# Kernel tuning notes

Measured on AMD Instinct MI355X. Metric: run time of the kernel, lower is better.

Reference implementation:

```python
import jax, jax.numpy as jnp
import numpy as np

B, C, D, O = 4, 4096, 1024, 1024
PROJ = 256
RANKS = [1, 2, 4, 8]
E = len(RANKS)
CLAMP_MAX = float(np.log(1.0 / 0.01))  # log(100)


def setup_inputs() -> dict:
    key = jax.random.key(0)
    ks = jax.random.split(key, 16)
    inp = {
        "x": jax.random.normal(ks[0], (B, C, D), dtype=jnp.float32),
        "W": jax.random.normal(ks[1], (O, D), dtype=jnp.float32) / np.sqrt(D),
        "Wp": jax.random.normal(ks[2], (PROJ, D), dtype=jnp.float32) / np.sqrt(D),
        "bp": jnp.zeros((PROJ,), dtype=jnp.float32),
        "sim": jax.random.normal(ks[3], (PROJ, E), dtype=jnp.float32) * 0.01,
        "temp": jnp.full((1,), np.log(1.0 / 0.5), dtype=jnp.float32),
    }
    for i, r in enumerate(RANKS):
        inp[f"Wd{i}"] = jax.random.normal(ks[4 + 2 * i], (r, D), dtype=jnp.float32) / r
        inp[f"Wu{i}"] = jax.random.normal(ks[5 + 2 * i], (O, r), dtype=jnp.float32) * 0.01
    return inp


def _l2norm(v, axis):
    return v / jnp.maximum(jnp.linalg.norm(v, axis=axis, keepdims=True), 1e-12)


def reference(x, W, Wp, bp, sim, temp, Wd0, Wu0, Wd1, Wu1, Wd2, Wu2, Wd3, Wu3):
    # base linear (bias=False)
    base = jnp.einsum("bcd,od->bco", x, W)

    # cosine top-k gate on flattened tokens
    xf = x.reshape(-1, x.shape[-1])                         # [N, D]
    proj = _l2norm(xf @ Wp.T + bp, axis=1)                  # [N, PROJ]
    simn = _l2norm(sim, axis=0)                             # [PROJ, E]
    scale = jnp.exp(jnp.minimum(temp, CLAMP_MAX))
    logits = (proj @ simn) * scale                          # [N, E]

    # eval mode: no noise. softmax then top-1 mask * prob
    lw = jax.nn.softmax(logits, axis=1)
    top1 = jnp.argmax(lw, axis=1)                           # [N]
    ret = jnp.where(jnp.arange(E)[None, :] == top1[:, None], lw, 0.0)
    ret = ret.reshape(x.shape[0], x.shape[1], E)            # [B, C, E]

    # dense per-expert LoRA (ranks differ, so small fixed loop)
    downs = (Wd0, Wd1, Wd2, Wd3)
    ups = (Wu0, Wu1, Wu2, Wu3)
    l = jnp.stack(
        [jnp.einsum("bcr,or->bco", jnp.einsum("bcd,rd->bcr", x, d), u)
         for d, u in zip(downs, ups)],
        axis=2,
    )                                                       # [B, C, E, O]
    res = jnp.sum(ret[..., None] * l, axis=2)               # [B, C, O]
    return base + res
```

## Files before the change

kernel.cpp:

```cpp
#include <hip/hip_runtime.h>

#define TOK 16384
#define DD 1024
#define OO 1024
#define KE 1088
#define NT 17
#define NB1 288
#define CLAMPV 4.605170185988091f

typedef __attribute__((ext_vector_type(8))) short short8;
typedef __attribute__((ext_vector_type(4))) float f32x4;

__device__ __forceinline__ unsigned short f2bf(float f) {
  unsigned int u = __float_as_uint(f);
  return (unsigned short)((u + 0x7FFFu + ((u >> 16) & 1u)) >> 16);
}

__device__ __forceinline__ void gload16(const unsigned short* g, unsigned short* l) {
  __builtin_amdgcn_global_load_lds(
      (const __attribute__((address_space(1))) void*)g,
      (__attribute__((address_space(3))) void*)l, 16, 0, 0);
}

__device__ __forceinline__ float down_val(int j, int d,
    const float* __restrict__ Wd0, const float* __restrict__ Wd1,
    const float* __restrict__ Wd2, const float* __restrict__ Wd3) {
  if (j == 0) return Wd0[d];
  if (j < 3) return Wd1[(j - 1) * DD + d];
  if (j < 7) return Wd2[(j - 3) * DD + d];
  if (j < 15) return Wd3[(j - 7) * DD + d];
  return 0.f;
}

__global__ __launch_bounds__(256) void prep3(
    const float* __restrict__ W, const float* __restrict__ Wp,
    const float* __restrict__ sim, const float* __restrict__ bp,
    const float* __restrict__ Wd0, const float* __restrict__ Wd1,
    const float* __restrict__ Wd2, const float* __restrict__ Wd3,
    const float* __restrict__ Wu0, const float* __restrict__ Wu1,
    const float* __restrict__ Wu2, const float* __restrict__ Wu3,
    unsigned short* __restrict__ Bx, unsigned short* __restrict__ B1,
    unsigned short* __restrict__ Ax, float* __restrict__ v4,
    float* __restrict__ c4) {
  __shared__ float simn_l[256][4];
  __shared__ float part[4][4];
  const int tid = threadIdx.x;
  if (blockIdx.x < 4) {
    float4 sv = *(const float4*)&sim[tid * 4];
    float v[4] = {sv.x * sv.x, sv.y * sv.y, sv.z * sv.z, sv.w * sv.w};
#pragma unroll
    for (int off = 1; off < 64; off <<= 1) {
#pragma unroll
      for (int e = 0; e < 4; ++e) v[e] += __shfl_xor(v[e], off, 64);
    }
    int wv = tid >> 6, ln = tid & 63;
    if (ln == 0) { part[wv][0] = v[0]; part[wv][1] = v[1]; part[wv][2] = v[2]; part[wv][3] = v[3]; }
    __syncthreads();
    float n0 = fmaxf(sqrtf(part[0][0] + part[1][0] + part[2][0] + part[3][0]), 1e-12f);
    float n1 = fmaxf(sqrtf(part[0][1] + part[1][1] + part[2][1] + part[3][1]), 1e-12f);
    float n2 = fmaxf(sqrtf(part[0][2] + part[1][2] + part[2][2] + part[3][2]), 1e-12f);
    float n3 = fmaxf(sqrtf(part[0][3] + part[1][3] + part[2][3] + part[3][3]), 1e-12f);
    simn_l[tid][0] = sv.x / n0; simn_l[tid][1] = sv.y / n1;
    simn_l[tid][2] = sv.z / n2; simn_l[tid][3] = sv.w / n3;
    __syncthreads();
    int d = blockIdx.x * 256 + tid;
    float a0 = 0.f, a1 = 0.f, a2 = 0.f, a3 = 0.f;
    for (int j = 0; j < 256; ++j) {
      float w = Wp[j * DD + d];
      a0 = __builtin_fmaf(w, simn_l[j][0], a0);
      a1 = __builtin_fmaf(w, simn_l[j][1], a1);
      a2 = __builtin_fmaf(w, simn_l[j][2], a2);
      a3 = __builtin_fmaf(w, simn_l[j][3], a3);
    }
    v4[d] = a0; v4[1024 + d] = a1; v4[2048 + d] = a2; v4[3072 + d] = a3;
    if (blockIdx.x == 0) {
      float bpv = bp[tid];
      float pc[4] = {simn_l[tid][0] * bpv, simn_l[tid][1] * bpv,
                     simn_l[tid][2] * bpv, simn_l[tid][3] * bpv};
#pragma unroll
      for (int off = 1; off < 64; off <<= 1) {
#pragma unroll
        for (int e = 0; e < 4; ++e) pc[e] += __shfl_xor(pc[e], off, 64);
      }
      __syncthreads();
      if (ln == 0) { part[wv][0] = pc[0]; part[wv][1] = pc[1]; part[wv][2] = pc[2]; part[wv][3] = pc[3]; }
      __syncthreads();
      if (tid == 0) {
#pragma unroll
        for (int e = 0; e < 4; ++e)
          c4[e] = part[0][e] + part[1][e] + part[2][e] + part[3][e];
      }
    }
  }
  const int nB1 = NB1 * DD;
  const int nWb = OO * KE;
  const int nXpad = TOK * 48;
  const int total = nB1 + nWb + nXpad;
  for (int i = blockIdx.x * 256 + tid; i < total; i += gridDim.x * 256) {
    if (i < nB1) {
      int r = i >> 10, c = i & 1023;
      float v = 0.f;
      if (r < 256) v = Wp[r * DD + c];
      else if (r < 271) v = down_val(r - 256, c, Wd0, Wd1, Wd2, Wd3);
      B1[i] = f2bf(v);
    } else if (i < nB1 + nWb) {
      int j = i - nB1;
      int o = j / KE, c = j - o * KE;
      float v = 0.f;
      if (c < 1024) v = W[o * DD + c];
      else if (c == 1024) v = Wu0[o];
      else if (c < 1027) v = Wu1[o * 2 + (c - 1025)];
      else if (c < 1031) v = Wu2[o * 4 + (c - 1027)];
      else if (c < 1039) v = Wu3[o * 8 + (c - 1031)];
      Bx[j] = f2bf(v);
    } else {
      int j = i - nB1 - nWb;
      int row = j / 48, c = j - row * 48;
      Ax[row * KE + 1040 + c] = 0;
    }
  }
}

__global__ __launch_bounds__(512, 1) void gemm2f(
    const float* __restrict__ x, const float* __restrict__ v4,
    unsigned short* __restrict__ Ax, const unsigned short* __restrict__ B1,
    const float* __restrict__ c4, const float* __restrict__ bp,
    const float* __restrict__ temp) {
  __shared__ __align__(16) unsigned short as1[2][64 * 32];
  __shared__ __align__(16) unsigned short bs1[2][NB1 * 32];
  __shared__ float ssq_s[2][64];
  __shared__ float xdown_s[64][16];
  __shared__ __align__(16) float dots_s[64][4];
  const int tid = threadIdx.x;
  const int lane = tid & 63, wv = tid >> 6;
  const int wm = wv >> 1, wn = wv & 1;
  const int r0 = blockIdx.x * 64;
  const int ro = lane & 15, ko = (lane >> 4) * 8;
  const int srow = lane >> 2, scol = (lane & 3) * 8;
  const int xr = tid >> 3;
  const int xc = (tid & 7) * 4;
  const float* xgp = &x[(r0 + xr) * DD + xc];
  unsigned short* axp = &Ax[(r0 + xr) * KE + xc];
  f32x4 acc[9] = {};
  float dotp[4] = {};
  float4 xv, va, vb, vc, vd;
  float4 xn, na, nb, nc, nd;

#define STB1(KT, BUF)                                                         \
  for (int c = wv; c < 18; c += 8)                                            \
    gload16(&B1[(c * 16 + srow) * DD + (KT) * 32 + scol], &bs1[BUF][c * 512]);

#define LOADX(KT, X, VA, VB, VC, VD) do {                                     \
    X  = *(const float4*)(xgp + (KT) * 32);                                   \
    VA = *(const float4*)&v4[(KT) * 32 + xc];                                 \
    VB = *(const float4*)&v4[1024 + (KT) * 32 + xc];                          \
    VC = *(const float4*)&v4[2048 + (KT) * 32 + xc];                          \
    VD = *(const float4*)&v4[3072 + (KT) * 32 + xc];                          \
  } while (0)

#define PROC(KT, BUF) do {                                                    \
    dotp[0] = __builtin_fmaf(xv.x, va.x, __builtin_fmaf(xv.y, va.y,           \
              __builtin_fmaf(xv.z, va.z, __builtin_fmaf(xv.w, va.w, dotp[0])))); \
    dotp[1] = __builtin_fmaf(xv.x, vb.x, __builtin_fmaf(xv.y, vb.y,           \
              __builtin_fmaf(xv.z, vb.z, __builtin_fmaf(xv.w, vb.w, dotp[1])))); \
    dotp[2] = __builtin_fmaf(xv.x, vc.x, __builtin_fmaf(xv.y, vc.y,           \
              __builtin_fmaf(xv.z, vc.z, __builtin_fmaf(xv.w, vc.w, dotp[2])))); \
    dotp[3] = __builtin_fmaf(xv.x, vd.x, __builtin_fmaf(xv.y, vd.y,           \
              __builtin_fmaf(xv.z, vd.z, __builtin_fmaf(xv.w, vd.w, dotp[3])))); \
    union { unsigned short s[4]; uint2 q; } pk;                               \
    pk.s[0] = f2bf(xv.x); pk.s[1] = f2bf(xv.y);                               \
    pk.s[2] = f2bf(xv.z); pk.s[3] = f2bf(xv.w);                               \
    *reinterpret_cast<uint2*>(axp + (KT) * 32) = pk.q;                        \
    *reinterpret_cast<uint2*>(&as1[BUF][xr * 32 + xc]) = pk.q;                \
  } while (0)

#define MM(BUF) do {                                                          \
    const unsigned short* ap = &as1[BUF][0];                                  \
    const unsigned short* bpp = &bs1[BUF][0];                                 \
    short8 af = *reinterpret_cast<const short8*>(ap + (wm * 16 + ro) * 32 + ko); \
    _Pragma("unroll")                                                         \
    for (int n = 0; n < 9; ++n) {                                             \
      short8 bf = *reinterpret_cast<const short8*>(                           \
          bpp + (wn * 144 + n * 16 + ro) * 32 + ko);                          \
      acc[n] = __builtin_amdgcn_mfma_f32_16x16x32_bf16(af, bf, acc[n], 0, 0, 0); \
    }                                                                         \
  } while (0)

  LOADX(0, xv, va, vb, vc, vd);
  STB1(0, 0)
  __builtin_amdgcn_sched_barrier(0);
  PROC(0, 0);
  LOADX(1, xn, na, nb, nc, nd);
  asm volatile("s_waitcnt vmcnt(6) lgkmcnt(0)" ::: "memory");
  __builtin_amdgcn_s_barrier();
  xv = xn; va = na; vb = nb; vc = nc; vd = nd;

  for (int u = 0; u < 32; ++u) {
    const int cb = u & 1;
    if (u < 31) {
      STB1(u + 1, cb ^ 1)
      __builtin_amdgcn_sched_barrier(0);
      PROC(u + 1, cb ^ 1);
      if (u < 30) LOADX(u + 2, xn, na, nb, nc, nd);
    }
    MM(cb);
    if (u < 31) {
      if (u < 30) {
        asm volatile("s_waitcnt vmcnt(6) lgkmcnt(0)" ::: "memory");
      } else {
        asm volatile("s_waitcnt vmcnt(1) lgkmcnt(0)" ::: "memory");
      }
      __builtin_amdgcn_s_barrier();
      xv = xn; va = na; vb = nb; vc = nc; vd = nd;
    }
  }

#pragma unroll
  for (int off = 1; off < 8; off <<= 1) {
#pragma unroll
    for (int e = 0; e < 4; ++e) dotp[e] += __shfl_xor(dotp[e], off, 64);
  }
  if ((lane & 7) == 0) {
    dots_s[xr][0] = dotp[0]; dots_s[xr][1] = dotp[1];
    dots_s[xr][2] = dotp[2]; dots_s[xr][3] = dotp[3];
  }

  float ssqp[4] = {};
#pragma unroll
  for (int n = 0; n < 9; ++n) {
    int col = wn * 144 + n * 16 + ro;
    if (col < 256) {
      float b = bp[col];
#pragma unroll
      for (int r = 0; r < 4; ++r) {
        float a = acc[n][r] + b;
        ssqp[r] = __builtin_fmaf(a, a, ssqp[r]);
      }
    }
  }
#pragma unroll
  for (int off = 1; off < 16; off <<= 1) {
#pragma unroll
    for (int r = 0; r < 4; ++r) ssqp[r] += __shfl_xor(ssqp[r], off, 64);
  }
  if (ro == 0) {
#pragma unroll
    for (int r = 0; r < 4; ++r)
      ssq_s[wn][wm * 16 + (lane >> 4) * 4 + r] = ssqp[r];
  }
  if (wn == 1 && ro < 15) {
#pragma unroll
    for (int r = 0; r < 4; ++r)
      xdown_s[wm * 16 + (lane >> 4) * 4 + r][ro] = acc[7][r];
  }
  __syncthreads();

  if (tid < 64) {
    const int row = tid, t = r0 + row;
    float ssqT = ssq_s[0][row] + ssq_s[1][row];
    float4 cc = *reinterpret_cast<const float4*>(c4);
    float scale = expf(fminf(temp[0], CLAMPV));
    float inv = scale / fmaxf(sqrtf(ssqT), 1e-12f);
    float l[4];
    l[0] = (dots_s[row][0] + cc.x) * inv; l[1] = (dots_s[row][1] + cc.y) * inv;
    l[2] = (dots_s[row][2] + cc.z) * inv; l[3] = (dots_s[row][3] + cc.w) * inv;
    int be = 0; float m = l[0];
    if (l[1] > m) { m = l[1]; be = 1; }
    if (l[2] > m) { m = l[2]; be = 2; }
    if (l[3] > m) { m = l[3]; be = 3; }
    float den = expf(l[0] - m) + expf(l[1] - m) + expf(l[2] - m) + expf(l[3] - m);
    float g = 1.0f / den;
    int off = (1 << be) - 1;
    int rr = 1 << be;
    union { unsigned short s[16]; uint4 v[2]; } o;
#pragma unroll
    for (int j = 0; j < 16; ++j) {
      float dv = xdown_s[row][j & 15];
      float v = (j >= off && j < off + rr) ? g * dv : 0.f;
      o.s[j] = f2bf(v);
    }
    uint4* dst = reinterpret_cast<uint4*>(&Ax[t * KE + 1024]);
    dst[0] = o.v[0];
    dst[1] = o.v[1];
  }
#undef STB1
#undef LOADX
#undef PROC
#undef MM
}

__global__ __launch_bounds__(512, 2) void main_gemm8(
    const unsigned short* __restrict__ A, const unsigned short* __restrict__ Bm,
    float* __restrict__ C) {
  __shared__ __align__(16) unsigned short lbuf[2][32768];
  const int tid = threadIdx.x;
  const int lane = tid & 63, wv = tid >> 6;
  const int wm = wv >> 2, wn = wv & 3;
  const int dd = blockIdx.x;
  const int tt = (dd & 7) * 32 + (dd >> 3);
  const int bx = tt & 3, by = tt >> 2;
  const int r0 = by * 256, c0 = bx * 256;
  const int ro = lane & 15, ko = (lane >> 4) * 8;
  const int rowb = ro * 128;
  const int swz = (ro & 7) << 4;
  const int lk0 = (ko * 2) ^ swz;
  const int lk1 = (64 + ko * 2) ^ swz;
  const int ll = (lane * 16) ^ ((lane >> 3) << 4);
  const int sro = ll >> 7;
  const int sk = (ll & 127) >> 1;
  f32x4 acc[8][4] = {};
  short8 Af[4][2], B0[2][2], B1r[2][2];

#define STG(MTX, GRB, HBU, BUF, U2)                                           \
  do {                                                                        \
    gload16(&MTX[((GRB) + (0 * 8 + wv) * 8 + sro) * KE + (U2) * 64 + sk],     \
            &lbuf[BUF][(HBU) + (0 * 8 + wv) * 512]);                          \
    gload16(&MTX[((GRB) + (1 * 8 + wv) * 8 + sro) * KE + (U2) * 64 + sk],     \
            &lbuf[BUF][(HBU) + (1 * 8 + wv) * 512]);                          \
  } while (0)

#define LDA(FI, QM, LK) (*reinterpret_cast<const short8*>(                    \
    (const char*)Ab + wm * 16384 + (QM) * 8192 + (FI) * 2048 + rowb + (LK)))
#define LDB(FN, QN, LK) (*reinterpret_cast<const short8*>(                    \
    (const char*)Bb + wn * 8192 + (QN) * 4096 + (FN) * 2048 + rowb + (LK)))

#define MMQ(QM, QN, BF)                                                       \
  do {                                                                        \
    _Pragma("unroll")                                                         \
    for (int fi = 0; fi < 4; ++fi) {                                          \
      _Pragma("unroll")                                                       \
      for (int fn = 0; fn < 2; ++fn) {                                        \
        acc[(QM)*4+fi][(QN)*2+fn] = __builtin_amdgcn_mfma_f32_16x16x32_bf16(  \
            Af[fi][0], BF[fn][0], acc[(QM)*4+fi][(QN)*2+fn], 0, 0, 0);        \
        acc[(QM)*4+fi][(QN)*2+fn] = __builtin_amdgcn_mfma_f32_16x16x32_bf16(  \
            Af[fi][1], BF[fn][1], acc[(QM)*4+fi][(QN)*2+fn], 0, 0, 0);        \
      }                                                                       \
    }                                                                         \
  } while (0)

  STG(Bm, c0,       16384, 0, 0);
  STG(A,  r0,       0,     0, 0);
  STG(Bm, c0 + 128, 24576, 0, 0);
  STG(A,  r0 + 128, 8192,  0, 0);
  STG(Bm, c0,       16384, 1, 1);
  STG(A,  r0,       0,     1, 1);
  asm volatile("s_waitcnt vmcnt(4)" ::: "memory");
  __builtin_amdgcn_s_barrier();

  for (int u = 0; u < NT; ++u) {
    const int db = u & 1;
    const unsigned short* Ab = &lbuf[db][0];
    const unsigned short* Bb = &lbuf[db][16384];
#pragma unroll
    for (int fi = 0; fi < 4; ++fi) { Af[fi][0] = LDA(fi, 0, lk0); Af[fi][1] = LDA(fi, 0, lk1); }
#pragma unroll
    for (int fn = 0; fn < 2; ++fn) { B0[fn][0] = LDB(fn, 0, lk0); B0[fn][1] = LDB(fn, 0, lk1); }
    if (u + 1 < NT) STG(Bm, c0 + 128, 24576, (u + 1) & 1, u + 1);
    __builtin_amdgcn_s_barrier();
    __builtin_amdgcn_s_setprio(1);
    MMQ(0, 0, B0);
    __builtin_amdgcn_s_setprio(0);
    __builtin_amdgcn_s_barrier();
#pragma unroll
    for (int fn = 0; fn < 2; ++fn) { B1r[fn][0] = LDB(fn, 1, lk0); B1r[fn][1] = LDB(fn, 1, lk1); }
    if (u + 1 < NT) STG(A, r0 + 128, 8192, (u + 1) & 1, u + 1);
    __builtin_amdgcn_s_barrier();
    __builtin_amdgcn_s_setprio(1);
    MMQ(0, 1, B1r);
    __builtin_amdgcn_s_setprio(0);
    __builtin_amdgcn_s_barrier();
#pragma unroll
    for (int fi = 0; fi < 4; ++fi) { Af[fi][0] = LDA(fi, 1, lk0); Af[fi][1] = LDA(fi, 1, lk1); }
    if (u + 2 < NT) STG(Bm, c0, 16384, db, u + 2);
    __builtin_amdgcn_s_barrier();
    __builtin_amdgcn_s_setprio(1);
    MMQ(1, 1, B1r);
    __builtin_amdgcn_s_setprio(0);
    __builtin_amdgcn_s_barrier();
    if (u + 2 < NT) STG(A, r0, 0, db, u + 2);
    __builtin_amdgcn_s_barrier();
    __builtin_amdgcn_s_setprio(1);
    MMQ(1, 0, B0);
    __builtin_amdgcn_s_setprio(0);
    if (u + 2 < NT) {
      asm volatile("s_waitcnt vmcnt(4)" ::: "memory");
    } else if (u == NT - 2) {
      asm volatile("s_waitcnt vmcnt(0)" ::: "memory");
    }
    __builtin_amdgcn_s_barrier();
  }

#pragma unroll
  for (int m = 0; m < 8; ++m) {
    int rr = r0 + wm * 128 + m * 16 + (lane >> 4) * 4;
#pragma unroll
    for (int n = 0; n < 4; ++n) {
      int cc = c0 + wn * 64 + n * 16 + ro;
#pragma unroll
      for (int v = 0; v < 4; ++v)
        C[(rr + v) * OO + cc] = acc[m][n][v];
    }
  }
#undef STG
#undef LDA
#undef LDB
#undef MMQ
}

extern "C" void kernel_launch(void* const* d_in, const int* in_sizes, int n_in,
                              void* d_out, int out_size, void* d_ws, size_t ws_size,
                              hipStream_t stream) {
  const float* x    = (const float*)d_in[0];
  const float* W    = (const float*)d_in[1];
  const float* Wp   = (const float*)d_in[2];
  const float* bp   = (const float*)d_in[3];
  const float* sim  = (const float*)d_in[4];
  const float* temp = (const float*)d_in[5];
  const float* Wd0  = (const float*)d_in[6];
  const float* Wu0  = (const float*)d_in[7];
  const float* Wd1  = (const float*)d_in[8];
  const float* Wu1  = (const float*)d_in[9];
  const float* Wd2  = (const float*)d_in[10];
  const float* Wu2  = (const float*)d_in[11];
  const float* Wd3  = (const float*)d_in[12];
  const float* Wu3  = (const float*)d_in[13];
  float* out = (float*)d_out;
  char* ws = (char*)d_ws;
  unsigned short* Ax  = (unsigned short*)ws;
  unsigned short* Bx  = (unsigned short*)(ws + 35651584);
  unsigned short* B1  = (unsigned short*)(ws + 37879808);
  float* v4           = (float*)(ws + 38469632);
  float* c4           = (float*)(ws + 38486016);

  prep3<<<1024, 256, 0, stream>>>(W, Wp, sim, bp, Wd0, Wd1, Wd2, Wd3,
                                  Wu0, Wu1, Wu2, Wu3, Bx, B1, Ax, v4, c4);
  gemm2f<<<256, 512, 0, stream>>>(x, v4, Ax, B1, c4, bp, temp);
  main_gemm8<<<256, 512, 0, stream>>>(Ax, Bx, out);
}
```

Baseline: 107.0 us.

## Halve gemm2f row tile to 32 rows with 256-thread blocks and simplify pipeline

Splits the projection/gate GEMM into 512 blocks of 256 threads, each covering 32 token rows instead of 64, so more blocks fill the 256 CUs and two can co-reside per CU. The hand-tuned register-prefetch pipeline with explicit waitcnt and s_barrier is replaced by a simpler load-then-use stage synchronised with __syncthreads. Each block now reloads the full B1 weight tile for half as many rows, doubling B1 traffic, and global-load latency for x is no longer hidden by a one-stage prefetch.

```diff
diff --git a/kernel.cpp b/kernel.cpp
--- a/kernel.cpp
+++ b/kernel.cpp
@@ -121,20 +121,20 @@
   }
 }
 
-__global__ __launch_bounds__(512, 1) void gemm2f(
+__global__ __launch_bounds__(256, 2) void gemm2f(
     const float* __restrict__ x, const float* __restrict__ v4,
     unsigned short* __restrict__ Ax, const unsigned short* __restrict__ B1,
     const float* __restrict__ c4, const float* __restrict__ bp,
     const float* __restrict__ temp) {
-  __shared__ __align__(16) unsigned short as1[2][64 * 32];
+  __shared__ __align__(16) unsigned short as1[2][32 * 32];
   __shared__ __align__(16) unsigned short bs1[2][NB1 * 32];
-  __shared__ float ssq_s[2][64];
-  __shared__ float xdown_s[64][16];
-  __shared__ __align__(16) float dots_s[64][4];
+  __shared__ float ssq_s[2][32];
+  __shared__ float xdown_s[32][16];
+  __shared__ __align__(16) float dots_s[32][4];
   const int tid = threadIdx.x;
   const int lane = tid & 63, wv = tid >> 6;
   const int wm = wv >> 1, wn = wv & 1;
-  const int r0 = blockIdx.x * 64;
+  const int r0 = blockIdx.x * 32;
   const int ro = lane & 15, ko = (lane >> 4) * 8;
   const int srow = lane >> 2, scol = (lane & 3) * 8;
   const int xr = tid >> 3;
@@ -143,22 +143,17 @@
   unsigned short* axp = &Ax[(r0 + xr) * KE + xc];
   f32x4 acc[9] = {};
   float dotp[4] = {};
-  float4 xv, va, vb, vc, vd;
-  float4 xn, na, nb, nc, nd;
 
 #define STB1(KT, BUF)                                                         \
-  for (int c = wv; c < 18; c += 8)                                            \
+  for (int c = wv; c < 18; c += 4)                                            \
     gload16(&B1[(c * 16 + srow) * DD + (KT) * 32 + scol], &bs1[BUF][c * 512]);
 
-#define LOADX(KT, X, VA, VB, VC, VD) do {                                     \
-    X  = *(const float4*)(xgp + (KT) * 32);                                   \
-    VA = *(const float4*)&v4[(KT) * 32 + xc];                                 \
-    VB = *(const float4*)&v4[1024 + (KT) * 32 + xc];                          \
-    VC = *(const float4*)&v4[2048 + (KT) * 32 + xc];                          \
-    VD = *(const float4*)&v4[3072 + (KT) * 32 + xc];                          \
-  } while (0)
-
-#define PROC(KT, BUF) do {                                                    \
+#define XSTG(KT, BUF) do {                                                    \
+    float4 xv = *(const float4*)(xgp + (KT) * 32);                            \
+    float4 va = *(const float4*)&v4[(KT) * 32 + xc];                          \
+    float4 vb = *(const float4*)&v4[1024 + (KT) * 32 + xc];                   \
+    float4 vc = *(const float4*)&v4[2048 + (KT) * 32 + xc];                   \
+    float4 vd = *(const float4*)&v4[3072 + (KT) * 32 + xc];                   \
     dotp[0] = __builtin_fmaf(xv.x, va.x, __builtin_fmaf(xv.y, va.y,           \
               __builtin_fmaf(xv.z, va.z, __builtin_fmaf(xv.w, va.w, dotp[0])))); \
     dotp[1] = __builtin_fmaf(xv.x, vb.x, __builtin_fmaf(xv.y, vb.y,           \
@@ -186,32 +181,19 @@
     }                                                                         \
   } while (0)
 
-  LOADX(0, xv, va, vb, vc, vd);
+  XSTG(0, 0);
   STB1(0, 0)
-  __builtin_amdgcn_sched_barrier(0);
-  PROC(0, 0);
-  LOADX(1, xn, na, nb, nc, nd);
-  asm volatile("s_waitcnt vmcnt(6) lgkmcnt(0)" ::: "memory");
-  __builtin_amdgcn_s_barrier();
-  xv = xn; va = na; vb = nb; vc = nc; vd = nd;
-
+  __syncthreads();
+  int cur = 0;
   for (int u = 0; u < 32; ++u) {
-    const int cb = u & 1;
     if (u < 31) {
-      STB1(u + 1, cb ^ 1)
-      __builtin_amdgcn_sched_barrier(0);
-      PROC(u + 1, cb ^ 1);
-      if (u < 30) LOADX(u + 2, xn, na, nb, nc, nd);
-    }
-    MM(cb);
+      XSTG(u + 1, cur ^ 1);
+      STB1(u + 1, cur ^ 1)
+    }
+    MM(cur);
     if (u < 31) {
-      if (u < 30) {
-        asm volatile("s_waitcnt vmcnt(6) lgkmcnt(0)" ::: "memory");
-      } else {
-        asm volatile("s_waitcnt vmcnt(1) lgkmcnt(0)" ::: "memory");
-      }
-      __builtin_amdgcn_s_barrier();
-      xv = xn; va = na; vb = nb; vc = nc; vd = nd;
+      __syncthreads();
+      cur ^= 1;
     }
   }
 
@@ -255,7 +237,7 @@
   }
   __syncthreads();
 
-  if (tid < 64) {
+  if (tid < 32) {
     const int row = tid, t = r0 + row;
     float ssqT = ssq_s[0][row] + ssq_s[1][row];
     float4 cc = *reinterpret_cast<const float4*>(c4);
@@ -284,8 +266,7 @@
     dst[1] = o.v[1];
   }
 #undef STB1
-#undef LOADX
-#undef PROC
+#undef XSTG
 #undef MM
 }
 
@@ -434,6 +415,6 @@
 
   prep3<<<1024, 256, 0, stream>>>(W, Wp, sim, bp, Wd0, Wd1, Wd2, Wd3,
                                   Wu0, Wu1, Wu2, Wu3, Bx, B1, Ax, v4, c4);
-  gemm2f<<<256, 512, 0, stream>>>(x, v4, Ax, B1, c4, bp, temp);
+  gemm2f<<<512, 256, 0, stream>>>(x, v4, Ax, B1, c4, bp, temp);
   main_gemm8<<<256, 512, 0, stream>>>(Ax, Bx, out);
 }
```

After: 107.4 us. About the same (+0.4%).
